# Performance work log

Hardware: AMD Instinct MI355X
Metric: run time of the kernel (lower is better)

The kernel has to match this reference:

```python
import jax, jax.numpy as jnp
import numpy as np

D_MODEL = 1024
NUM_LATENTS = 8
N_HEADS = 8
HEAD_DIM = D_MODEL // N_HEADS
LN_EPS = 1e-5
NEG_INF = -1e9


def setup_inputs() -> dict:
    key = jax.random.key(0)
    ks = jax.random.split(key, 9)
    B, S, d = 8, 8192, D_MODEL
    hidden_states = jax.random.normal(ks[0], (B, S, d), dtype=jnp.float32)
    attention_mask = jax.random.randint(ks[1], (B, S), 0, 2, dtype=jnp.int32)
    # guarantee at least one valid token per row
    attention_mask = attention_mask.at[:, 0].set(1)
    latent_queries = jax.random.normal(ks[2], (NUM_LATENTS, d), dtype=jnp.float32) * 0.02
    lim = 1.0 / np.sqrt(d)
    in_proj_weight = jax.random.uniform(ks[3], (3 * d, d), minval=-lim, maxval=lim, dtype=jnp.float32)
    in_proj_bias = jnp.zeros((3 * d,), jnp.float32)
    out_proj_weight = jax.random.uniform(ks[4], (d, d), minval=-lim, maxval=lim, dtype=jnp.float32)
    out_proj_bias = jnp.zeros((d,), jnp.float32)
    ln_gamma = jnp.ones((d,), jnp.float32)
    ln_beta = jnp.zeros((d,), jnp.float32)
    return {
        "hidden_states": hidden_states,
        "latent_queries": latent_queries,
        "in_proj_weight": in_proj_weight,
        "in_proj_bias": in_proj_bias,
        "out_proj_weight": out_proj_weight,
        "out_proj_bias": out_proj_bias,
        "ln_gamma": ln_gamma,
        "ln_beta": ln_beta,
        "attention_mask": attention_mask,
    }


def reference(hidden_states, latent_queries, in_proj_weight, in_proj_bias,
              out_proj_weight, out_proj_bias, ln_gamma, ln_beta, attention_mask):
    B, S, d = hidden_states.shape
    K, H, hd = NUM_LATENTS, N_HEADS, HEAD_DIM
    Wq, Wk, Wv = jnp.split(in_proj_weight, 3, axis=0)   # each [d, d]
    bq, bk, bv = jnp.split(in_proj_bias, 3, axis=0)
    # projections (queries shared over batch)
    q = latent_queries @ Wq.T + bq                      # [K, d]
    k = hidden_states @ Wk.T + bk                       # [B, S, d]
    v = hidden_states @ Wv.T + bv                       # [B, S, d]
    q = q.reshape(K, H, hd).transpose(1, 0, 2)          # [H, K, hd]
    k = k.reshape(B, S, H, hd).transpose(0, 2, 1, 3)    # [B, H, S, hd]
    v = v.reshape(B, S, H, hd).transpose(0, 2, 1, 3)    # [B, H, S, hd]
    scale = 1.0 / np.sqrt(hd)
    scores = jnp.einsum('hkd,bhsd->bhks', q, k) * scale  # [B, H, K, S]
    pad = (attention_mask == 0)[:, None, None, :]        # [B, 1, 1, S]
    scores = jnp.where(pad, NEG_INF, scores)
    attn = jax.nn.softmax(scores, axis=-1)
    ctx = jnp.einsum('bhks,bhsd->bhkd', attn, v)         # [B, H, K, hd]
    ctx = ctx.transpose(0, 2, 1, 3).reshape(B, K, d)     # [B, K, d]
    pooled = ctx @ out_proj_weight.T + out_proj_bias     # [B, K, d]
    # LayerNorm
    mu = pooled.mean(-1, keepdims=True)
    var = jnp.mean(jnp.square(pooled - mu), axis=-1, keepdims=True)
    pooled = (pooled - mu) * jax.lax.rsqrt(var + LN_EPS) * ln_gamma + ln_beta
    return pooled.mean(axis=1)                           # [B, d]
```

## Files before the change

kernel.cpp:

```cpp
#include <hip/hip_runtime.h>
#include <math.h>

#define D_M 1024
#define S_L 8192
#define B_N 8
#define H_N 8
#define HD_ 128
#define HK_ 64
#define SCALE_ 0.08838834764831845f
#define NEG_INF_ -1e9f
#define PITCH_ 40
#define AP_ 72

typedef _Float16 half8v __attribute__((ext_vector_type(8)));
typedef _Float16 half4v __attribute__((ext_vector_type(4)));
typedef float floatx4 __attribute__((ext_vector_type(4)));

__global__ void k_q(const float* __restrict__ lat, const float* __restrict__ W,
                    const float* __restrict__ bias, float* __restrict__ q) {
  int g = blockIdx.x * blockDim.x + threadIdx.x;
  int kidx = g >> 10, i = g & 1023;
  const float* wr = W + (size_t)i * D_M;
  const float* lr = lat + kidx * D_M;
  float acc = bias[i];
  #pragma unroll 4
  for (int t = 0; t < D_M; t += 4) {
    float4 w = *(const float4*)(wr + t);
    float4 l = *(const float4*)(lr + t);
    acc += w.x*l.x + w.y*l.y + w.z*l.z + w.w*l.w;
  }
  q[g] = acc;
}

__global__ void k_qt(const float* __restrict__ q, const float* __restrict__ W,
                     const float* __restrict__ bias, _Float16* __restrict__ qth,
                     float* __restrict__ qconst) {
  int g = blockIdx.x * blockDim.x + threadIdx.x;
  int hk = g >> 10, j = g & 1023;
  int h = hk >> 3, kidx = hk & 7;
  const float* qr = q + kidx * D_M + h * HD_;
  const float* wb = W + ((size_t)D_M + (size_t)h * HD_) * D_M + j;
  float acc = 0.f;
  #pragma unroll 4
  for (int dd = 0; dd < HD_; ++dd)
    acc += qr[dd] * wb[(size_t)dd * D_M];
  qth[g] = (_Float16)(acc * SCALE_);
  if (j == 0) {
    const float* bk = bias + D_M + h * HD_;
    float c = 0.f;
    for (int dd = 0; dd < HD_; ++dd) c += qr[dd] * bk[dd];
    qconst[hk] = c * SCALE_;
  }
}

__global__ __launch_bounds__(256, 4) void k_scores3(
    const float* __restrict__ hsrc, const _Float16* __restrict__ qth,
    const float* __restrict__ qc, const int* __restrict__ mask,
    _Float16* __restrict__ ph, float* __restrict__ pm, float* __restrict__ pl) {
  __shared__ __align__(16) _Float16 As[128 * AP_];
  __shared__ __align__(16) _Float16 Bs[64 * AP_];
  __shared__ int smask[128];
  __shared__ float qcs[64];
  const int tid = threadIdx.x;
  const int b = blockIdx.x >> 6;
  const int st = blockIdx.x & 63;
  const int s0 = st * 128;
  const int w = tid >> 6, l = tid & 63;
  const int row16 = l & 15, kc = l >> 4;
  if (tid < 128) smask[tid] = mask[b * S_L + s0 + tid];
  if (tid < 64) qcs[tid] = qc[tid];
  floatx4 acc[2][4];
  #pragma unroll
  for (int mf = 0; mf < 2; ++mf)
    #pragma unroll
    for (int nf = 0; nf < 4; ++nf) acc[mf][nf] = (floatx4){0.f, 0.f, 0.f, 0.f};

  const int r_ = tid >> 3, c_ = tid & 7;
  const float* hb = hsrc + ((size_t)b * S_L + s0) * D_M;
  float4 fa[4][2];
  half8v fb[2];
  #pragma unroll
  for (int p = 0; p < 4; ++p) {
    const float* pr = hb + (size_t)(p * 32 + r_) * D_M + c_ * 8;
    fa[p][0] = *(const float4*)pr; fa[p][1] = *(const float4*)(pr + 4);
  }
  fb[0] = *(const half8v*)(qth + (size_t)r_ * D_M + c_ * 8);
  fb[1] = *(const half8v*)(qth + (size_t)(r_ + 32) * D_M + c_ * 8);

  for (int k0 = 0; k0 < D_M; k0 += 64) {
    __syncthreads();
    #pragma unroll
    for (int p = 0; p < 4; ++p) {
      half8v hv;
      hv[0] = (_Float16)fa[p][0].x; hv[1] = (_Float16)fa[p][0].y;
      hv[2] = (_Float16)fa[p][0].z; hv[3] = (_Float16)fa[p][0].w;
      hv[4] = (_Float16)fa[p][1].x; hv[5] = (_Float16)fa[p][1].y;
      hv[6] = (_Float16)fa[p][1].z; hv[7] = (_Float16)fa[p][1].w;
      *(half8v*)&As[(p * 32 + r_) * AP_ + c_ * 8] = hv;
    }
    *(half8v*)&Bs[r_ * AP_ + c_ * 8] = fb[0];
    *(half8v*)&Bs[(r_ + 32) * AP_ + c_ * 8] = fb[1];
    if (k0 + 64 < D_M) {
      #pragma unroll
      for (int p = 0; p < 4; ++p) {
        const float* pr = hb + (size_t)(p * 32 + r_) * D_M + (k0 + 64) + c_ * 8;
        fa[p][0] = *(const float4*)pr; fa[p][1] = *(const float4*)(pr + 4);
      }
      fb[0] = *(const half8v*)(qth + (size_t)r_ * D_M + (k0 + 64) + c_ * 8);
      fb[1] = *(const half8v*)(qth + (size_t)(r_ + 32) * D_M + (k0 + 64) + c_ * 8);
    }
    __syncthreads();
    #pragma unroll
    for (int kk = 0; kk < 2; ++kk) {
      half8v af[2], bf4[4];
      #pragma unroll
      for (int mf = 0; mf < 2; ++mf)
        af[mf] = *(const half8v*)&As[(w * 32 + mf * 16 + row16) * AP_ + kk * 32 + kc * 8];
      #pragma unroll
      for (int nf = 0; nf < 4; ++nf)
        bf4[nf] = *(const half8v*)&Bs[(nf * 16 + row16) * AP_ + kk * 32 + kc * 8];
      #pragma unroll
      for (int mf = 0; mf < 2; ++mf)
        #pragma unroll
        for (int nf = 0; nf < 4; ++nf)
          acc[mf][nf] = __builtin_amdgcn_mfma_f32_16x16x32_f16(af[mf], bf4[nf], acc[mf][nf], 0, 0, 0);
    }
  }
  __syncthreads();
  _Float16 (*pT)[68] = (_Float16 (*)[68])As;
  int msk[8];
  #pragma unroll
  for (int mf = 0; mf < 2; ++mf)
    #pragma unroll
    for (int r = 0; r < 4; ++r)
      msk[mf * 4 + r] = smask[w * 32 + mf * 16 + kc * 4 + r];
  #pragma unroll
  for (int nf = 0; nf < 4; ++nf) {
    int hk = nf * 16 + row16;
    float qcv = qcs[hk];
    float vals[8];
    float mloc = -3.4e38f;
    #pragma unroll
    for (int mf = 0; mf < 2; ++mf)
      #pragma unroll
      for (int r = 0; r < 4; ++r) {
        float v = msk[mf * 4 + r] ? (acc[mf][nf][r] + qcv) : NEG_INF_;
        vals[mf * 4 + r] = v;
        mloc = fmaxf(mloc, v);
      }
    mloc = fmaxf(mloc, __shfl_xor(mloc, 16, 64));
    mloc = fmaxf(mloc, __shfl_xor(mloc, 32, 64));
    float ls = 0.f;
    #pragma unroll
    for (int mf = 0; mf < 2; ++mf)
      #pragma unroll
      for (int r = 0; r < 4; ++r) {
        float e = __expf(vals[mf * 4 + r] - mloc);
        ls += e;
        pT[w * 32 + mf * 16 + kc * 4 + r][hk] = (_Float16)e;
      }
    ls += __shfl_xor(ls, 16, 64);
    ls += __shfl_xor(ls, 32, 64);
    if (kc == 0) {
      int idx = ((b * 64 + st) * 4 + w) * 64 + hk;
      pm[idx] = mloc;
      pl[idx] = ls;
    }
  }
  __syncthreads();
  {
    int hk2 = tid >> 2, q4 = tid & 3;
    _Float16* dst = ph + ((size_t)b * 64 + hk2) * S_L + s0 + q4 * 32;
    #pragma unroll
    for (int i = 0; i < 4; ++i) {
      half8v v;
      #pragma unroll
      for (int e = 0; e < 8; ++e) v[e] = pT[q4 * 32 + i * 8 + e][hk2];
      *(half8v*)(dst + i * 8) = v;
    }
  }
}

__global__ __launch_bounds__(256) void k_stats2c(
    const float* __restrict__ pm, const float* __restrict__ pl,
    float* __restrict__ lvinv, float* __restrict__ sf) {
  __shared__ float red[256];
  int bh = blockIdx.x;
  int b = bh >> 6, hk = bh & 63;
  int tid = threadIdx.x;
  float m = pm[((size_t)b * 256 + tid) * 64 + hk];
  float lv = pl[((size_t)b * 256 + tid) * 64 + hk];
  red[tid] = m; __syncthreads();
  for (int off = 128; off > 0; off >>= 1) {
    if (tid < off) red[tid] = fmaxf(red[tid], red[tid + off]);
    __syncthreads();
  }
  float M = red[0]; __syncthreads();
  float f = __expf(m - M);
  red[tid] = lv * f; __syncthreads();
  for (int off = 128; off > 0; off >>= 1) {
    if (tid < off) red[tid] += red[tid + off];
    __syncthreads();
  }
  if (tid == 0) lvinv[bh] = 1.f / red[0];
  sf[(size_t)bh * 256 + tid] = f;
}

__global__ __launch_bounds__(512) void k_part(
    const float* __restrict__ hsrc, const _Float16* __restrict__ ph,
    const float* __restrict__ sf, float* __restrict__ part) {
  __shared__ __align__(16) _Float16 htile[512 * PITCH_];
  const int tid = threadIdx.x;
  const int b  = blockIdx.x >> 5;
  const int jb = (blockIdx.x >> 4) & 1;
  const int sc = blockIdx.x & 15;
  const int w = tid >> 6, l = tid & 63;
  const int row16 = l & 15, kc = l >> 4;
  const int s_base = sc * 512;
  const float* hb = hsrc + (size_t)b * S_L * D_M + jb * 512;
  const _Float16* phb = ph + (size_t)b * HK_ * S_L;
  const float* sfb = sf + (size_t)b * HK_ * 256;
  floatx4 acc[4][4];
  #pragma unroll
  for (int mf = 0; mf < 4; ++mf)
    #pragma unroll
    for (int nf = 0; nf < 4; ++nf) acc[mf][nf] = (floatx4){0.f, 0.f, 0.f, 0.f};

  const int jcol = tid;
  float colv[32];
  #pragma unroll
  for (int s = 0; s < 32; ++s)
    colv[s] = hb[(size_t)(s_base + s) * D_M + jcol];

  for (int t = 0; t < 16; ++t) {
    const int s0 = s_base + t * 32;
    __syncthreads();
    #pragma unroll
    for (int sb = 0; sb < 8; ++sb) {
      half4v hv;
      hv[0] = (_Float16)colv[sb * 4 + 0];
      hv[1] = (_Float16)colv[sb * 4 + 1];
      hv[2] = (_Float16)colv[sb * 4 + 2];
      hv[3] = (_Float16)colv[sb * 4 + 3];
      *(half4v*)&htile[jcol * PITCH_ + sb * 4] = hv;
    }
    __syncthreads();
    if (t < 15) {
      #pragma unroll
      for (int s = 0; s < 32; ++s)
        colv[s] = hb[(size_t)(s0 + 32 + s) * D_M + jcol];
    }
    const int t32 = sc * 16 + t;
    half8v ap[4];
    #pragma unroll
    for (int mf = 0; mf < 4; ++mf) {
      half8v raw = *(const half8v*)(phb + (size_t)(mf * 16 + row16) * S_L + s0 + kc * 8);
      _Float16 fv = (_Float16)sfb[(size_t)(mf * 16 + row16) * 256 + t32];
      #pragma unroll
      for (int e = 0; e < 8; ++e) ap[mf][e] = raw[e] * fv;
    }
    #pragma unroll
    for (int nf = 0; nf < 4; ++nf) {
      int j = w * 64 + nf * 16 + row16;
      half8v bv = *(const half8v*)&htile[j * PITCH_ + kc * 8];
      #pragma unroll
      for (int mf = 0; mf < 4; ++mf)
        acc[mf][nf] = __builtin_amdgcn_mfma_f32_16x16x32_f16(ap[mf], bv, acc[mf][nf], 0, 0, 0);
    }
  }
  #pragma unroll
  for (int mf = 0; mf < 4; ++mf)
    #pragma unroll
    for (int nf = 0; nf < 4; ++nf) {
      int j = w * 64 + nf * 16 + row16;
      #pragma unroll
      for (int r = 0; r < 4; ++r) {
        int hk = mf * 16 + kc * 4 + r;
        part[(((size_t)(b * 2 + jb) * 16 + sc) * HK_ + hk) * 512 + j] = acc[mf][nf][r];
      }
    }
}

__global__ void k_comb(const float* __restrict__ part, const float* __restrict__ lvinv,
                       float* __restrict__ ctxh) {
  int g = blockIdx.x * blockDim.x + threadIdx.x;
  int b = g >> 14;
  int rem = g & 16383;
  int hk = rem >> 8;
  int j4 = rem & 255;
  int jb = j4 >> 7;
  int jr4 = j4 & 127;
  const float* pb = part + ((size_t)(b * 2 + jb) * 16 * HK_ + hk) * 512 + jr4 * 4;
  float4 s = make_float4(0.f, 0.f, 0.f, 0.f);
  #pragma unroll
  for (int sc = 0; sc < 16; ++sc) {
    float4 v = *(const float4*)(pb + (size_t)sc * HK_ * 512);
    s.x += v.x; s.y += v.y; s.z += v.z; s.w += v.w;
  }
  float li = lvinv[b * 64 + hk];
  s.x *= li; s.y *= li; s.z *= li; s.w *= li;
  *(float4*)(ctxh + ((size_t)b * HK_ + hk) * D_M + j4 * 4) = s;
}

__global__ void k_ctx(const float* __restrict__ ctxh, const float* __restrict__ W,
                      const float* __restrict__ bias, float* __restrict__ ctx) {
  int g2 = blockIdx.x * blockDim.x + threadIdx.x;
  int o = g2 >> 2, kq = g2 & 3;
  int b = o >> 13, kidx = (o >> 10) & 7, i = o & 1023;
  int hk = (i >> 7) * 8 + kidx;
  const float* wr = W + ((size_t)2 * D_M + i) * D_M + kq * 256;
  const float* xr = ctxh + ((size_t)b * HK_ + hk) * D_M + kq * 256;
  float acc = 0.f;
  #pragma unroll 8
  for (int t = 0; t < 256; t += 4) {
    float4 w = *(const float4*)(wr + t);
    float4 x = *(const float4*)(xr + t);
    acc += w.x*x.x + w.y*x.y + w.z*x.z + w.w*x.w;
  }
  acc += __shfl_xor(acc, 1, 64);
  acc += __shfl_xor(acc, 2, 64);
  if (kq == 0) ctx[o] = acc + bias[2 * D_M + i];
}

__global__ void k_pool(const float* __restrict__ ctx, const float* __restrict__ W,
                       const float* __restrict__ bias, float* __restrict__ pooled) {
  int g2 = blockIdx.x * blockDim.x + threadIdx.x;
  int o = g2 >> 2, kq = g2 & 3;
  int b = o >> 13, kidx = (o >> 10) & 7, i = o & 1023;
  const float* wr = W + (size_t)i * D_M + kq * 256;
  const float* xr = ctx + ((size_t)b * 8 + kidx) * D_M + kq * 256;
  float acc = 0.f;
  #pragma unroll 8
  for (int t = 0; t < 256; t += 4) {
    float4 w = *(const float4*)(wr + t);
    float4 x = *(const float4*)(xr + t);
    acc += w.x*x.x + w.y*x.y + w.z*x.z + w.w*x.w;
  }
  acc += __shfl_xor(acc, 1, 64);
  acc += __shfl_xor(acc, 2, 64);
  if (kq == 0) pooled[o] = acc + bias[i];
}

__global__ void k_ln(const float* __restrict__ pooled, const float* __restrict__ gamma,
                     const float* __restrict__ beta, float* __restrict__ out) {
  __shared__ float red[256];
  int b = blockIdx.x, tid = threadIdx.x;
  float acc[4] = {0.f, 0.f, 0.f, 0.f};
  for (int kidx = 0; kidx < 8; ++kidx) {
    const float* row = pooled + ((size_t)b * 8 + kidx) * D_M;
    float v[4]; float s = 0.f;
    #pragma unroll
    for (int c = 0; c < 4; ++c) { v[c] = row[tid + 256 * c]; s += v[c]; }
    red[tid] = s; __syncthreads();
    for (int off = 128; off > 0; off >>= 1) {
      if (tid < off) red[tid] += red[tid + off];
      __syncthreads();
    }
    float mu = red[0] * (1.f / 1024.f);
    __syncthreads();
    float ss = 0.f;
    #pragma unroll
    for (int c = 0; c < 4; ++c) { float dd = v[c] - mu; ss += dd * dd; }
    red[tid] = ss; __syncthreads();
    for (int off = 128; off > 0; off >>= 1) {
      if (tid < off) red[tid] += red[tid + off];
      __syncthreads();
    }
    float rstd = rsqrtf(red[0] * (1.f / 1024.f) + 1e-5f);
    __syncthreads();
    #pragma unroll
    for (int c = 0; c < 4; ++c) {
      int i = tid + 256 * c;
      acc[c] += ((v[c] - mu) * rstd * gamma[i] + beta[i]) * 0.125f;
    }
  }
  #pragma unroll
  for (int c = 0; c < 4; ++c) out[(size_t)b * D_M + tid + 256 * c] = acc[c];
}

extern "C" void kernel_launch(void* const* d_in, const int* in_sizes, int n_in,
                              void* d_out, int out_size, void* d_ws, size_t ws_size,
                              hipStream_t stream) {
  const float* hidden = (const float*)d_in[0];
  const float* latent = (const float*)d_in[1];
  const float* w_in   = (const float*)d_in[2];
  const float* b_in   = (const float*)d_in[3];
  const float* w_out  = (const float*)d_in[4];
  const float* b_out  = (const float*)d_in[5];
  const float* gamma  = (const float*)d_in[6];
  const float* beta   = (const float*)d_in[7];
  const int*   mask   = (const int*)d_in[8];
  float* out = (float*)d_out;
  float* ws = (float*)d_ws;
  float* q      = ws;
  float* qc     = q + 8192;
  float* lvinv  = qc + 64;
  float* pm     = lvinv + 512;
  float* pl     = pm + 131072;
  float* sf     = pl + 131072;
  _Float16* qth = (_Float16*)(sf + 131072);
  _Float16* ph  = (_Float16*)(sf + 131072 + 32768);
  float* part   = sf + 131072 + 32768 + 2097152;
  float* ctxh   = part + 8388608;
  float* ctx    = ctxh + 524288;
  float* pooled = ctx + 65536;

  k_q       <<<32,   256, 0, stream>>>(latent, w_in, b_in, q);
  k_qt      <<<256,  256, 0, stream>>>(q, w_in, b_in, qth, qc);
  k_scores3 <<<512,  256, 0, stream>>>(hidden, qth, qc, mask, ph, pm, pl);
  k_stats2c <<<512,  256, 0, stream>>>(pm, pl, lvinv, sf);
  k_part    <<<256,  512, 0, stream>>>(hidden, ph, sf, part);
  k_comb    <<<512,  256, 0, stream>>>(part, lvinv, ctxh);
  k_ctx     <<<1024, 256, 0, stream>>>(ctxh, w_in, b_in, ctx);
  k_pool    <<<1024, 256, 0, stream>>>(ctx, w_out, b_out, pooled);
  k_ln      <<<8,    256, 0, stream>>>(pooled, gamma, beta, out);
}
```

Before: 323.3 us.

## Read pre-swizzled query fragments from global and double-buffer the A tile

k_qt now writes the scaled query-key product in a fragment-major layout, so k_scores3 can load B operands for MFMA straight from global (L2-resident) memory instead of staging them through shared memory. The A tile becomes double-buffered in LDS, which removes one __syncthreads per k-step, and the launch-bounds occupancy hint is dropped. The aim is less LDS traffic and fewer barriers in the score GEMM. The cost is more global loads per wave, and the looser launch bounds may change register allocation and occupancy.

```diff
diff --git a/kernel.cpp b/kernel.cpp
--- a/kernel.cpp
+++ b/kernel.cpp
@@ -33,7 +33,7 @@
 }
 
 __global__ void k_qt(const float* __restrict__ q, const float* __restrict__ W,
-                     const float* __restrict__ bias, _Float16* __restrict__ qth,
+                     const float* __restrict__ bias, _Float16* __restrict__ qtr,
                      float* __restrict__ qconst) {
   int g = blockIdx.x * blockDim.x + threadIdx.x;
   int hk = g >> 10, j = g & 1023;
@@ -44,7 +44,7 @@
   #pragma unroll 4
   for (int dd = 0; dd < HD_; ++dd)
     acc += qr[dd] * wb[(size_t)dd * D_M];
-  qth[g] = (_Float16)(acc * SCALE_);
+  qtr[((j >> 3) * 64 + hk) * 8 + (j & 7)] = (_Float16)(acc * SCALE_);
   if (j == 0) {
     const float* bk = bias + D_M + h * HD_;
     float c = 0.f;
@@ -53,12 +53,11 @@
   }
 }
 
-__global__ __launch_bounds__(256, 4) void k_scores3(
-    const float* __restrict__ hsrc, const _Float16* __restrict__ qth,
+__global__ __launch_bounds__(256) void k_scores3(
+    const float* __restrict__ hsrc, const _Float16* __restrict__ qtr,
     const float* __restrict__ qc, const int* __restrict__ mask,
     _Float16* __restrict__ ph, float* __restrict__ pm, float* __restrict__ pl) {
-  __shared__ __align__(16) _Float16 As[128 * AP_];
-  __shared__ __align__(16) _Float16 Bs[64 * AP_];
+  __shared__ __align__(16) _Float16 As[2][128 * AP_];
   __shared__ int smask[128];
   __shared__ float qcs[64];
   const int tid = threadIdx.x;
@@ -77,18 +76,15 @@
 
   const int r_ = tid >> 3, c_ = tid & 7;
   const float* hb = hsrc + ((size_t)b * S_L + s0) * D_M;
+  const _Float16* br = qtr + (size_t)(kc * 64) * 8 + row16 * 8;
   float4 fa[4][2];
-  half8v fb[2];
   #pragma unroll
   for (int p = 0; p < 4; ++p) {
     const float* pr = hb + (size_t)(p * 32 + r_) * D_M + c_ * 8;
     fa[p][0] = *(const float4*)pr; fa[p][1] = *(const float4*)(pr + 4);
   }
-  fb[0] = *(const half8v*)(qth + (size_t)r_ * D_M + c_ * 8);
-  fb[1] = *(const half8v*)(qth + (size_t)(r_ + 32) * D_M + c_ * 8);
-
+  int cur = 0;
   for (int k0 = 0; k0 < D_M; k0 += 64) {
-    __syncthreads();
     #pragma unroll
     for (int p = 0; p < 4; ++p) {
       half8v hv;
@@ -96,38 +92,33 @@
       hv[2] = (_Float16)fa[p][0].z; hv[3] = (_Float16)fa[p][0].w;
       hv[4] = (_Float16)fa[p][1].x; hv[5] = (_Float16)fa[p][1].y;
       hv[6] = (_Float16)fa[p][1].z; hv[7] = (_Float16)fa[p][1].w;
-      *(half8v*)&As[(p * 32 + r_) * AP_ + c_ * 8] = hv;
-    }
-    *(half8v*)&Bs[r_ * AP_ + c_ * 8] = fb[0];
-    *(half8v*)&Bs[(r_ + 32) * AP_ + c_ * 8] = fb[1];
+      *(half8v*)&As[cur][(p * 32 + r_) * AP_ + c_ * 8] = hv;
+    }
+    __syncthreads();
     if (k0 + 64 < D_M) {
       #pragma unroll
       for (int p = 0; p < 4; ++p) {
         const float* pr = hb + (size_t)(p * 32 + r_) * D_M + (k0 + 64) + c_ * 8;
         fa[p][0] = *(const float4*)pr; fa[p][1] = *(const float4*)(pr + 4);
       }
-      fb[0] = *(const half8v*)(qth + (size_t)r_ * D_M + (k0 + 64) + c_ * 8);
-      fb[1] = *(const half8v*)(qth + (size_t)(r_ + 32) * D_M + (k0 + 64) + c_ * 8);
-    }
-    __syncthreads();
+    }
     #pragma unroll
     for (int kk = 0; kk < 2; ++kk) {
-      half8v af[2], bf4[4];
-      #pragma unroll
-      for (int mf = 0; mf < 2; ++mf)
-        af[mf] = *(const half8v*)&As[(w * 32 + mf * 16 + row16) * AP_ + kk * 32 + kc * 8];
-      #pragma unroll
-      for (int nf = 0; nf < 4; ++nf)
-        bf4[nf] = *(const half8v*)&Bs[(nf * 16 + row16) * AP_ + kk * 32 + kc * 8];
-      #pragma unroll
-      for (int mf = 0; mf < 2; ++mf)
-        #pragma unroll
-        for (int nf = 0; nf < 4; ++nf)
-          acc[mf][nf] = __builtin_amdgcn_mfma_f32_16x16x32_f16(af[mf], bf4[nf], acc[mf][nf], 0, 0, 0);
-    }
+      half8v af[2];
+      af[0] = *(const half8v*)&As[cur][(w * 32 + row16) * AP_ + kk * 32 + kc * 8];
+      af[1] = *(const half8v*)&As[cur][(w * 32 + 16 + row16) * AP_ + kk * 32 + kc * 8];
+      const _Float16* bq = br + (size_t)(k0 / 32 + kk) * 2048;
+      #pragma unroll
+      for (int nf = 0; nf < 4; ++nf) {
+        half8v bf = *(const half8v*)(bq + nf * 128);
+        acc[0][nf] = __builtin_amdgcn_mfma_f32_16x16x32_f16(af[0], bf, acc[0][nf], 0, 0, 0);
+        acc[1][nf] = __builtin_amdgcn_mfma_f32_16x16x32_f16(af[1], bf, acc[1][nf], 0, 0, 0);
+      }
+    }
+    cur ^= 1;
   }
   __syncthreads();
-  _Float16 (*pT)[68] = (_Float16 (*)[68])As;
+  _Float16 (*pT)[68] = (_Float16 (*)[68])&As[0][0];
   int msk[8];
   #pragma unroll
   for (int mf = 0; mf < 2; ++mf)
@@ -398,7 +389,7 @@
   float* pm     = lvinv + 512;
   float* pl     = pm + 131072;
   float* sf     = pl + 131072;
-  _Float16* qth = (_Float16*)(sf + 131072);
+  _Float16* qtr = (_Float16*)(sf + 131072);
   _Float16* ph  = (_Float16*)(sf + 131072 + 32768);
   float* part   = sf + 131072 + 32768 + 2097152;
   float* ctxh   = part + 8388608;
@@ -406,8 +397,8 @@
   float* pooled = ctx + 65536;
 
   k_q       <<<32,   256, 0, stream>>>(latent, w_in, b_in, q);
-  k_qt      <<<256,  256, 0, stream>>>(q, w_in, b_in, qth, qc);
-  k_scores3 <<<512,  256, 0, stream>>>(hidden, qth, qc, mask, ph, pm, pl);
+  k_qt      <<<256,  256, 0, stream>>>(q, w_in, b_in, qtr, qc);
+  k_scores3 <<<512,  256, 0, stream>>>(hidden, qtr, qc, mask, ph, pm, pl);
   k_stats2c <<<512,  256, 0, stream>>>(pm, pl, lvinv, sf);
   k_part    <<<256,  512, 0, stream>>>(hidden, ph, sf, part);
   k_comb    <<<512,  256, 0, stream>>>(part, lvinv, ctxh);
```

Result: slower. 337.5 us (+4.4%).

## Stream scores-kernel tiles straight into LDS with double-buffered async loads

Applied to the files above, without the earlier changes.

Rewrites the k_scores3 main loop so fp32 hidden-state and fp16 query tiles go directly from global memory to LDS using global_load_lds. The tiles are double-buffered with a 32-wide K step, and an XOR swizzle applied on the global side avoids bank conflicts. The fp32 to fp16 conversion moves from the staging registers to the LDS read side, and the occupancy hint is dropped from launch_bounds. The aim is to cut register staging and overlap the next tile's load with the MFMA work, at the cost of twice as much LDS traffic for the fp32 A tile and reliance on correct wait handling for the async LDS writes.

```diff
diff --git a/kernel.cpp b/kernel.cpp
--- a/kernel.cpp
+++ b/kernel.cpp
@@ -10,11 +10,16 @@
 #define SCALE_ 0.08838834764831845f
 #define NEG_INF_ -1e9f
 #define PITCH_ 40
-#define AP_ 72
+#define BK_ 32
 
 typedef _Float16 half8v __attribute__((ext_vector_type(8)));
 typedef _Float16 half4v __attribute__((ext_vector_type(4)));
 typedef float floatx4 __attribute__((ext_vector_type(4)));
+
+#define GLL16(gp, lp)                                                          \
+  __builtin_amdgcn_global_load_lds(                                            \
+      (const __attribute__((address_space(1))) unsigned int*)(gp),             \
+      (__attribute__((address_space(3))) unsigned int*)(lp), 16, 0, 0)
 
 __global__ void k_q(const float* __restrict__ lat, const float* __restrict__ W,
                     const float* __restrict__ bias, float* __restrict__ q) {
@@ -53,12 +58,12 @@
   }
 }
 
-__global__ __launch_bounds__(256, 4) void k_scores3(
+__global__ __launch_bounds__(256) void k_scores3(
     const float* __restrict__ hsrc, const _Float16* __restrict__ qth,
     const float* __restrict__ qc, const int* __restrict__ mask,
     _Float16* __restrict__ ph, float* __restrict__ pm, float* __restrict__ pl) {
-  __shared__ __align__(16) _Float16 As[128 * AP_];
-  __shared__ __align__(16) _Float16 Bs[64 * AP_];
+  __shared__ __align__(16) float Asb[2][128 * BK_];
+  __shared__ __align__(16) _Float16 Bsb[2][64 * BK_];
   __shared__ int smask[128];
   __shared__ float qcs[64];
   const int tid = threadIdx.x;
@@ -75,59 +80,61 @@
     #pragma unroll
     for (int nf = 0; nf < 4; ++nf) acc[mf][nf] = (floatx4){0.f, 0.f, 0.f, 0.f};
 
-  const int r_ = tid >> 3, c_ = tid & 7;
   const float* hb = hsrc + ((size_t)b * S_L + s0) * D_M;
-  float4 fa[4][2];
-  half8v fb[2];
-  #pragma unroll
-  for (int p = 0; p < 4; ++p) {
-    const float* pr = hb + (size_t)(p * 32 + r_) * D_M + c_ * 8;
-    fa[p][0] = *(const float4*)pr; fa[p][1] = *(const float4*)(pr + 4);
-  }
-  fb[0] = *(const half8v*)(qth + (size_t)r_ * D_M + c_ * 8);
-  fb[1] = *(const half8v*)(qth + (size_t)(r_ + 32) * D_M + c_ * 8);
-
-  for (int k0 = 0; k0 < D_M; k0 += 64) {
-    __syncthreads();
-    #pragma unroll
-    for (int p = 0; p < 4; ++p) {
-      half8v hv;
-      hv[0] = (_Float16)fa[p][0].x; hv[1] = (_Float16)fa[p][0].y;
-      hv[2] = (_Float16)fa[p][0].z; hv[3] = (_Float16)fa[p][0].w;
-      hv[4] = (_Float16)fa[p][1].x; hv[5] = (_Float16)fa[p][1].y;
-      hv[6] = (_Float16)fa[p][1].z; hv[7] = (_Float16)fa[p][1].w;
-      *(half8v*)&As[(p * 32 + r_) * AP_ + c_ * 8] = hv;
-    }
-    *(half8v*)&Bs[r_ * AP_ + c_ * 8] = fb[0];
-    *(half8v*)&Bs[(r_ + 32) * AP_ + c_ * 8] = fb[1];
-    if (k0 + 64 < D_M) {
-      #pragma unroll
-      for (int p = 0; p < 4; ++p) {
-        const float* pr = hb + (size_t)(p * 32 + r_) * D_M + (k0 + 64) + c_ * 8;
-        fa[p][0] = *(const float4*)pr; fa[p][1] = *(const float4*)(pr + 4);
-      }
-      fb[0] = *(const half8v*)(qth + (size_t)r_ * D_M + (k0 + 64) + c_ * 8);
-      fb[1] = *(const half8v*)(qth + (size_t)(r_ + 32) * D_M + (k0 + 64) + c_ * 8);
-    }
-    __syncthreads();
-    #pragma unroll
-    for (int kk = 0; kk < 2; ++kk) {
-      half8v af[2], bf4[4];
-      #pragma unroll
-      for (int mf = 0; mf < 2; ++mf)
-        af[mf] = *(const half8v*)&As[(w * 32 + mf * 16 + row16) * AP_ + kk * 32 + kc * 8];
+
+  int ar_[4], ag_[4];
+  #pragma unroll
+  for (int i = 0; i < 4; ++i) {
+    int c = (w * 4 + i) * 64 + l;
+    ar_[i] = c >> 3;
+    ag_[i] = (c & 7) ^ (ar_[i] & 7);
+  }
+  const int bc_ = w * 64 + l;
+  const int br_ = bc_ >> 2;
+  const int bg_ = (bc_ & 3) ^ ((br_ >> 1) & 3);
+
+  #define STAGE_(buf, k0)                                                      \
+    do {                                                                       \
+      _Pragma("unroll")                                                        \
+      for (int i = 0; i < 4; ++i)                                              \
+        GLL16(hb + (size_t)ar_[i] * D_M + (k0) + ag_[i] * 4,                   \
+              &Asb[buf][(w * 4 + i) * 256]);                                   \
+      GLL16(qth + (size_t)br_ * D_M + (k0) + bg_ * 8, &Bsb[buf][w * 512]);     \
+    } while (0)
+
+  STAGE_(0, 0);
+  __syncthreads();
+  int cur = 0;
+  for (int k0 = 0; k0 < D_M; k0 += BK_) {
+    if (k0 + BK_ < D_M) STAGE_(cur ^ 1, k0 + BK_);
+    half8v af[2], bf4[4];
+    #pragma unroll
+    for (int mf = 0; mf < 2; ++mf) {
+      int row = w * 32 + mf * 16 + row16;
+      int ss0 = (kc * 2) ^ (row & 7);
+      int ss1 = (kc * 2 + 1) ^ (row & 7);
+      floatx4 a0 = *(const floatx4*)&Asb[cur][row * BK_ + ss0 * 4];
+      floatx4 a1 = *(const floatx4*)&Asb[cur][row * BK_ + ss1 * 4];
+      af[mf][0] = (_Float16)a0[0]; af[mf][1] = (_Float16)a0[1];
+      af[mf][2] = (_Float16)a0[2]; af[mf][3] = (_Float16)a0[3];
+      af[mf][4] = (_Float16)a1[0]; af[mf][5] = (_Float16)a1[1];
+      af[mf][6] = (_Float16)a1[2]; af[mf][7] = (_Float16)a1[3];
+    }
+    #pragma unroll
+    for (int nf = 0; nf < 4; ++nf) {
+      int row = nf * 16 + row16;
+      int ss = kc ^ ((row >> 1) & 3);
+      bf4[nf] = *(const half8v*)&Bsb[cur][row * BK_ + ss * 8];
+    }
+    #pragma unroll
+    for (int mf = 0; mf < 2; ++mf)
       #pragma unroll
       for (int nf = 0; nf < 4; ++nf)
-        bf4[nf] = *(const half8v*)&Bs[(nf * 16 + row16) * AP_ + kk * 32 + kc * 8];
-      #pragma unroll
-      for (int mf = 0; mf < 2; ++mf)
-        #pragma unroll
-        for (int nf = 0; nf < 4; ++nf)
-          acc[mf][nf] = __builtin_amdgcn_mfma_f32_16x16x32_f16(af[mf], bf4[nf], acc[mf][nf], 0, 0, 0);
-    }
-  }
-  __syncthreads();
-  _Float16 (*pT)[68] = (_Float16 (*)[68])As;
+        acc[mf][nf] = __builtin_amdgcn_mfma_f32_16x16x32_f16(af[mf], bf4[nf], acc[mf][nf], 0, 0, 0);
+    __syncthreads();
+    cur ^= 1;
+  }
+  _Float16 (*pT)[68] = (_Float16 (*)[68])&Asb[0][0];
   int msk[8];
   #pragma unroll
   for (int mf = 0; mf < 2; ++mf)
```

Result: no change. 324.8 us (+0.5%).
